# Kernel tuning notes

Measured on AMD Instinct MI355X. Metric: run time of the kernel, lower is better.

## Reference

```python
import jax, jax.numpy as jnp
import numpy as np

CR = 32  # channels // reduction

def setup_inputs() -> dict:
    key = jax.random.key(0)
    k1, k2 = jax.random.split(key)
    x = jax.random.normal(k1, (1, 64, 8, 32, 32), dtype=jnp.float32)
    W = jax.random.normal(k2, (CR, 64), dtype=jnp.float32) * (1.0 / np.sqrt(64.0))
    bias = jnp.zeros((CR,), dtype=jnp.float32)
    return {"x": x, "W": W, "bias": bias}

def reference(x, W, bias):
    b, c, d, h, w = x.shape
    cr = W.shape[0]
    n = d * h * w
    # 1x1x1 Conv3d == per-voxel linear projection over channels
    x_red = jnp.einsum('oc,bcdhw->bodhw', W, x) + bias[None, :, None, None, None]
    q = x_red.reshape(b, cr, n)          # [b, cr, N]
    k = q                                 # shared projection (q == k)
    v = x.reshape(b, c, n)               # [b, c, N]
    # attn[b, i, j] = <q[:, i], k[:, j]>, softmax over j (dim=2)
    attn = jnp.einsum('bci,bcj->bij', q, k) / jnp.sqrt(jnp.float32(cr))
    attn = jax.nn.softmax(attn, axis=2)
    # out[b, c, m] = sum_n v[b, c, n] * attn[b, n, m]  (torch.bmm(v, attn))
    out = jnp.einsum('bcn,bnm->bcm', v, attn)
    out = out.reshape(b, c, d, h, w)
    return out + x
```

## Files before the change

kernel.cpp:

```cpp
#include <hip/hip_runtime.h>

#define N_TOK 8192

typedef _Float16 f16x8 __attribute__((ext_vector_type(8)));
typedef _Float16 f16x4 __attribute__((ext_vector_type(4)));
typedef float    f32x4 __attribute__((ext_vector_type(4)));

__device__ __forceinline__ f32x4 mfma16(f16x8 a, f16x8 b, f32x4 c) {
  return __builtin_amdgcn_mfma_f32_16x16x32_f16(a, b, c, 0, 0, 0);
}

#define QSCALE 0.50500977f

__global__ __launch_bounds__(256) void prep_kernel(
    const float* __restrict__ x, const float* __restrict__ W,
    const float* __restrict__ bias, _Float16* __restrict__ qe,
    _Float16* __restrict__ vh) {
  int blk = blockIdx.x, t = threadIdx.x;
  if (blk < 1024) {
    __shared__ float Wl[32 * 65];
    for (int i = t; i < 2048; i += 256) Wl[(i >> 6) * 65 + (i & 63)] = W[i];
    __syncthreads();
    int g = blk * 256 + t;
    int o = g & 31, n = g >> 5;
    float acc0 = bias[o], acc1 = 0.f;
#pragma unroll
    for (int c = 0; c < 32; ++c) {
      acc0 = fmaf(Wl[o * 65 + c], x[c * N_TOK + n], acc0);
      acc1 = fmaf(Wl[o * 65 + 32 + c], x[(32 + c) * N_TOK + n], acc1);
    }
    qe[n * 32 + o] = (_Float16)((acc0 + acc1) * QSCALE);
  } else {
    int i4 = (blk - 1024) * 256 + t;
    f32x4 v = ((const f32x4*)x)[i4];
    f16x4 h;
#pragma unroll
    for (int j = 0; j < 4; ++j) h[j] = (_Float16)v[j];
    *(f16x4*)(vh + i4 * 4) = h;
  }
}

__global__ __launch_bounds__(512) void pass1_kernel(
    const _Float16* __restrict__ qe, float* __restrict__ Bn) {
  __shared__ float Lp[8][32];
  int t = threadIdx.x;
  int w = t >> 6, lane = t & 63, quad = lane >> 4, l15 = lane & 15;
  int n0 = blockIdx.x * 32;
  f16x8 af0 = *(const f16x8*)(qe + (n0 + l15) * 32 + quad * 8);
  f16x8 af1 = *(const f16x8*)(qe + (n0 + 16 + l15) * 32 + quad * 8);
  f32x4 sums0 = {0.f, 0.f, 0.f, 0.f}, sums1 = {0.f, 0.f, 0.f, 0.f};
  for (int mt = 0; mt < 64; ++mt) {
    int m0 = w * 1024 + mt * 16;
    f16x8 bf = *(const f16x8*)(qe + (m0 + l15) * 32 + quad * 8);
    f32x4 zero = {0.f, 0.f, 0.f, 0.f};
    f32x4 s0 = mfma16(af0, bf, zero);
    f32x4 s1 = mfma16(af1, bf, zero);
#pragma unroll
    for (int r = 0; r < 4; ++r) {
      sums0[r] += __builtin_amdgcn_exp2f(s0[r]);
      sums1[r] += __builtin_amdgcn_exp2f(s1[r]);
    }
  }
#pragma unroll
  for (int r = 0; r < 4; ++r) {
#pragma unroll
    for (int mask = 1; mask < 16; mask <<= 1) {
      sums0[r] += __shfl_xor(sums0[r], mask, 64);
      sums1[r] += __shfl_xor(sums1[r], mask, 64);
    }
  }
  if (l15 == 0) {
    *(f32x4*)&Lp[w][quad * 4] = sums0;
    *(f32x4*)&Lp[w][16 + quad * 4] = sums1;
  }
  __syncthreads();
  if (t < 32) {
    float L = 0.f;
#pragma unroll
    for (int ww = 0; ww < 8; ++ww) L += Lp[ww][t];
    Bn[n0 + t] = __builtin_amdgcn_logf(L);
  }
}

__global__ __launch_bounds__(1024) void pass2_kernel(
    const _Float16* __restrict__ qe, const _Float16* __restrict__ vh,
    const float* __restrict__ Bn, const float* __restrict__ x,
    float* __restrict__ out) {
  __shared__ _Float16 Pt[16 * 1280];
  __shared__ float Ot[8 * 64 * 33];
  int t = threadIdx.x;
  int w = t >> 6, lane = t & 63, quad = lane >> 4, l15 = lane & 15;
  int m0 = blockIdx.x * 32;
  _Float16* myP = Pt + w * 1280;

  f16x8 bm0 = *(const f16x8*)(qe + (m0 + l15) * 32 + quad * 8);
  f16x8 bm1 = *(const f16x8*)(qe + (m0 + 16 + l15) * 32 + quad * 8);

  f32x4 acc[4][2];
#pragma unroll
  for (int ct = 0; ct < 4; ++ct)
#pragma unroll
    for (int mt = 0; mt < 2; ++mt) acc[ct][mt] = f32x4{0.f, 0.f, 0.f, 0.f};

  for (int ch = 0; ch < 16; ++ch) {
    int nb = w * 512 + ch * 32;
    f16x8 an[2];
    an[0] = *(const f16x8*)(qe + (nb + l15) * 32 + quad * 8);
    an[1] = *(const f16x8*)(qe + (nb + 16 + l15) * 32 + quad * 8);
    f32x4 Bq[2];
    Bq[0] = *(const f32x4*)(Bn + nb + quad * 4);
    Bq[1] = *(const f32x4*)(Bn + nb + 16 + quad * 4);
    __asm__ volatile("s_waitcnt lgkmcnt(0)" ::: "memory");
#pragma unroll
    for (int nt = 0; nt < 2; ++nt) {
      f16x8 a = an[nt];
#pragma unroll
      for (int mt = 0; mt < 2; ++mt) {
        f32x4 zero = {0.f, 0.f, 0.f, 0.f};
        f32x4 s = mfma16(a, (mt == 0) ? bm0 : bm1, zero);
        f16x4 p;
#pragma unroll
        for (int r = 0; r < 4; ++r)
          p[r] = (_Float16)__builtin_amdgcn_exp2f(s[r] - Bq[nt][r]);
        *(f16x4*)(myP + (mt * 16 + l15) * 40 + nt * 16 + quad * 4) = p;
      }
    }
    __asm__ volatile("s_waitcnt lgkmcnt(0)" ::: "memory");
    f16x8 bp0 = *(const f16x8*)(myP + l15 * 40 + quad * 8);
    f16x8 bp1 = *(const f16x8*)(myP + (16 + l15) * 40 + quad * 8);
#pragma unroll
    for (int ct = 0; ct < 4; ++ct) {
      f16x8 av = *(const f16x8*)(vh + (ct * 16 + l15) * N_TOK + nb + quad * 8);
      acc[ct][0] = mfma16(av, bp0, acc[ct][0]);
      acc[ct][1] = mfma16(av, bp1, acc[ct][1]);
    }
  }

  if (w < 8) {
#pragma unroll
    for (int ct = 0; ct < 4; ++ct)
#pragma unroll
      for (int mt = 0; mt < 2; ++mt)
#pragma unroll
        for (int r = 0; r < 4; ++r)
          Ot[(w * 64 + ct * 16 + quad * 4 + r) * 33 + mt * 16 + l15] =
              acc[ct][mt][r];
  }
  __syncthreads();
  if (w >= 8) {
#pragma unroll
    for (int ct = 0; ct < 4; ++ct)
#pragma unroll
      for (int mt = 0; mt < 2; ++mt)
#pragma unroll
        for (int r = 0; r < 4; ++r)
          Ot[((w - 8) * 64 + ct * 16 + quad * 4 + r) * 33 + mt * 16 + l15] +=
              acc[ct][mt][r];
  }
  __syncthreads();
  for (int idx = t; idx < 2048; idx += 1024) {
    int cc = idx >> 5, m = idx & 31;
    float v = 0.f;
#pragma unroll
    for (int s = 0; s < 8; ++s) v += Ot[(s * 64 + cc) * 33 + m];
    out[cc * N_TOK + m0 + m] = v + x[cc * N_TOK + m0 + m];
  }
}

extern "C" void kernel_launch(void* const* d_in, const int* in_sizes, int n_in,
                              void* d_out, int out_size, void* d_ws,
                              size_t ws_size, hipStream_t stream) {
  const float* x = (const float*)d_in[0];
  const float* W = (const float*)d_in[1];
  const float* bias = (const float*)d_in[2];
  float* out = (float*)d_out;

  char* ws = (char*)d_ws;
  _Float16* qe = (_Float16*)ws;
  _Float16* vh = (_Float16*)(ws + 524288);
  float* Bn = (float*)(ws + 524288 + 1048576);

  prep_kernel<<<1536, 256, 0, stream>>>(x, W, bias, qe, vh);
  pass1_kernel<<<256, 512, 0, stream>>>(qe, Bn);
  pass2_kernel<<<256, 1024, 0, stream>>>(qe, vh, Bn, x, out);
}
```

Before: 113.9 us.

## Fuse prep and both attention passes into one cooperative kernel with grid syncs

Merges the three launches (projection/convert, log-sum-exp pass, output pass) into a single cooperative kernel of 256 blocks of 1024 threads, separated by grid-wide syncs. V is stored in a pre-permuted fp16 layout so the output pass can feed probabilities straight from the score MFMA registers into 16x16x16 MFMAs, removing the LDS round trip for P. Both passes also prefetch their next operand tiles into registers. The aim is to cut launch gaps and LDS traffic, at the cost of grid-sync overhead and a requirement that all 256 blocks be co-resident.

```diff
diff --git a/kernel.cpp b/kernel.cpp
--- a/kernel.cpp
+++ b/kernel.cpp
@@ -1,27 +1,39 @@
 #include <hip/hip_runtime.h>
+#include <hip/hip_cooperative_groups.h>
+
+namespace cg = cooperative_groups;
 
 #define N_TOK 8192
 
 typedef _Float16 f16x8 __attribute__((ext_vector_type(8)));
 typedef _Float16 f16x4 __attribute__((ext_vector_type(4)));
+typedef _Float16 f16x2 __attribute__((ext_vector_type(2)));
 typedef float    f32x4 __attribute__((ext_vector_type(4)));
 
-__device__ __forceinline__ f32x4 mfma16(f16x8 a, f16x8 b, f32x4 c) {
+__device__ __forceinline__ f32x4 mfma_k32(f16x8 a, f16x8 b, f32x4 c) {
   return __builtin_amdgcn_mfma_f32_16x16x32_f16(a, b, c, 0, 0, 0);
 }
+__device__ __forceinline__ f32x4 mfma_k16(f16x4 a, f16x4 b, f32x4 c) {
+  return __builtin_amdgcn_mfma_f32_16x16x16f16(a, b, c, 0, 0, 0);
+}
 
 #define QSCALE 0.50500977f
 
-__global__ __launch_bounds__(256) void prep_kernel(
+__global__ __launch_bounds__(1024, 4) void mega_kernel(
     const float* __restrict__ x, const float* __restrict__ W,
     const float* __restrict__ bias, _Float16* __restrict__ qe,
-    _Float16* __restrict__ vh) {
-  int blk = blockIdx.x, t = threadIdx.x;
-  if (blk < 1024) {
-    __shared__ float Wl[32 * 65];
-    for (int i = t; i < 2048; i += 256) Wl[(i >> 6) * 65 + (i & 63)] = W[i];
-    __syncthreads();
-    int g = blk * 256 + t;
+    _Float16* __restrict__ vp, float* __restrict__ Bn,
+    float* __restrict__ out) {
+  __shared__ float smem[8 * 64 * 33];
+  cg::grid_group grid = cg::this_grid();
+  int t = threadIdx.x, blk = blockIdx.x;
+  int w = t >> 6, lane = t & 63, quad = lane >> 4, l15 = lane & 15;
+
+  {
+    float* Wl = smem;
+    for (int i = t; i < 2048; i += 1024) Wl[(i >> 6) * 65 + (i & 63)] = W[i];
+    __syncthreads();
+    int g = blk * 1024 + t;
     int o = g & 31, n = g >> 5;
     float acc0 = bias[o], acc1 = 0.f;
 #pragma unroll
@@ -30,140 +42,157 @@
       acc1 = fmaf(Wl[o * 65 + 32 + c], x[(32 + c) * N_TOK + n], acc1);
     }
     qe[n * 32 + o] = (_Float16)((acc0 + acc1) * QSCALE);
-  } else {
-    int i4 = (blk - 1024) * 256 + t;
-    f32x4 v = ((const f32x4*)x)[i4];
-    f16x4 h;
-#pragma unroll
-    for (int j = 0; j < 4; ++j) h[j] = (_Float16)v[j];
-    *(f16x4*)(vh + i4 * 4) = h;
+    int f = g * 2;
+    int c = f >> 13, n2 = f & 8191;
+    float2 xv = *(const float2*)(x + f);
+    int gg = n2 >> 5, off = n2 & 31;
+    int nt = off >> 4, q2 = (off >> 2) & 3, j = off & 3;
+    f16x2 h;
+    h[0] = (_Float16)xv.x;
+    h[1] = (_Float16)xv.y;
+    *(f16x2*)(vp + ((gg * 64 + c) * 4 + q2) * 8 + nt * 4 + j) = h;
   }
-}
-
-__global__ __launch_bounds__(512) void pass1_kernel(
-    const _Float16* __restrict__ qe, float* __restrict__ Bn) {
-  __shared__ float Lp[8][32];
-  int t = threadIdx.x;
-  int w = t >> 6, lane = t & 63, quad = lane >> 4, l15 = lane & 15;
-  int n0 = blockIdx.x * 32;
-  f16x8 af0 = *(const f16x8*)(qe + (n0 + l15) * 32 + quad * 8);
-  f16x8 af1 = *(const f16x8*)(qe + (n0 + 16 + l15) * 32 + quad * 8);
-  f32x4 sums0 = {0.f, 0.f, 0.f, 0.f}, sums1 = {0.f, 0.f, 0.f, 0.f};
-  for (int mt = 0; mt < 64; ++mt) {
-    int m0 = w * 1024 + mt * 16;
-    f16x8 bf = *(const f16x8*)(qe + (m0 + l15) * 32 + quad * 8);
-    f32x4 zero = {0.f, 0.f, 0.f, 0.f};
-    f32x4 s0 = mfma16(af0, bf, zero);
-    f32x4 s1 = mfma16(af1, bf, zero);
+  grid.sync();
+
+  {
+    float(*Lp)[32] = reinterpret_cast<float(*)[32]>(smem);
+    int n0 = blk * 32;
+    f16x8 af0 = *(const f16x8*)(qe + (n0 + l15) * 32 + quad * 8);
+    f16x8 af1 = *(const f16x8*)(qe + (n0 + 16 + l15) * 32 + quad * 8);
+    const _Float16* qb = qe + (w * 512 + l15) * 32 + quad * 8;
+    f16x8 pb0 = *(const f16x8*)(qb);
+    f16x8 pb1 = *(const f16x8*)(qb + 512);
+    f32x4 a00 = {0.f, 0.f, 0.f, 0.f}, a01 = a00, a10 = a00, a11 = a00;
+    for (int mt = 0; mt < 16; ++mt) {
+      f16x8 b0 = pb0, b1 = pb1;
+      int nx = ((mt + 1) & 15) * 1024;
+      pb0 = *(const f16x8*)(qb + nx);
+      pb1 = *(const f16x8*)(qb + nx + 512);
+      f32x4 z = {0.f, 0.f, 0.f, 0.f};
+      f32x4 s00 = mfma_k32(af0, b0, z);
+      f32x4 s01 = mfma_k32(af0, b1, z);
+      f32x4 s10 = mfma_k32(af1, b0, z);
+      f32x4 s11 = mfma_k32(af1, b1, z);
+#pragma unroll
+      for (int r = 0; r < 4; ++r) {
+        a00[r] += __builtin_amdgcn_exp2f(s00[r]);
+        a01[r] += __builtin_amdgcn_exp2f(s01[r]);
+        a10[r] += __builtin_amdgcn_exp2f(s10[r]);
+        a11[r] += __builtin_amdgcn_exp2f(s11[r]);
+      }
+    }
+    f32x4 sums0 = a00 + a01;
+    f32x4 sums1 = a10 + a11;
 #pragma unroll
     for (int r = 0; r < 4; ++r) {
-      sums0[r] += __builtin_amdgcn_exp2f(s0[r]);
-      sums1[r] += __builtin_amdgcn_exp2f(s1[r]);
+#pragma unroll
+      for (int mask = 1; mask < 16; mask <<= 1) {
+        sums0[r] += __shfl_xor(sums0[r], mask, 64);
+        sums1[r] += __shfl_xor(sums1[r], mask, 64);
+      }
+    }
+    if (l15 == 0) {
+      *(f32x4*)&Lp[w][quad * 4] = sums0;
+      *(f32x4*)&Lp[w][16 + quad * 4] = sums1;
+    }
+    __syncthreads();
+    if (t < 32) {
+      float L = 0.f;
+#pragma unroll
+      for (int ww = 0; ww < 16; ++ww) L += Lp[ww][t];
+      Bn[n0 + t] = __builtin_amdgcn_logf(L);
     }
   }
-#pragma unroll
-  for (int r = 0; r < 4; ++r) {
-#pragma unroll
-    for (int mask = 1; mask < 16; mask <<= 1) {
-      sums0[r] += __shfl_xor(sums0[r], mask, 64);
-      sums1[r] += __shfl_xor(sums1[r], mask, 64);
-    }
-  }
-  if (l15 == 0) {
-    *(f32x4*)&Lp[w][quad * 4] = sums0;
-    *(f32x4*)&Lp[w][16 + quad * 4] = sums1;
-  }
-  __syncthreads();
-  if (t < 32) {
-    float L = 0.f;
-#pragma unroll
-    for (int ww = 0; ww < 8; ++ww) L += Lp[ww][t];
-    Bn[n0 + t] = __builtin_amdgcn_logf(L);
-  }
-}
-
-__global__ __launch_bounds__(1024) void pass2_kernel(
-    const _Float16* __restrict__ qe, const _Float16* __restrict__ vh,
-    const float* __restrict__ Bn, const float* __restrict__ x,
-    float* __restrict__ out) {
-  __shared__ _Float16 Pt[16 * 1280];
-  __shared__ float Ot[8 * 64 * 33];
-  int t = threadIdx.x;
-  int w = t >> 6, lane = t & 63, quad = lane >> 4, l15 = lane & 15;
-  int m0 = blockIdx.x * 32;
-  _Float16* myP = Pt + w * 1280;
-
-  f16x8 bm0 = *(const f16x8*)(qe + (m0 + l15) * 32 + quad * 8);
-  f16x8 bm1 = *(const f16x8*)(qe + (m0 + 16 + l15) * 32 + quad * 8);
-
-  f32x4 acc[4][2];
-#pragma unroll
-  for (int ct = 0; ct < 4; ++ct)
-#pragma unroll
-    for (int mt = 0; mt < 2; ++mt) acc[ct][mt] = f32x4{0.f, 0.f, 0.f, 0.f};
-
-  for (int ch = 0; ch < 16; ++ch) {
-    int nb = w * 512 + ch * 32;
-    f16x8 an[2];
-    an[0] = *(const f16x8*)(qe + (nb + l15) * 32 + quad * 8);
-    an[1] = *(const f16x8*)(qe + (nb + 16 + l15) * 32 + quad * 8);
-    f32x4 Bq[2];
-    Bq[0] = *(const f32x4*)(Bn + nb + quad * 4);
-    Bq[1] = *(const f32x4*)(Bn + nb + 16 + quad * 4);
-    __asm__ volatile("s_waitcnt lgkmcnt(0)" ::: "memory");
-#pragma unroll
-    for (int nt = 0; nt < 2; ++nt) {
-      f16x8 a = an[nt];
-#pragma unroll
-      for (int mt = 0; mt < 2; ++mt) {
-        f32x4 zero = {0.f, 0.f, 0.f, 0.f};
-        f32x4 s = mfma16(a, (mt == 0) ? bm0 : bm1, zero);
-        f16x4 p;
-#pragma unroll
-        for (int r = 0; r < 4; ++r)
-          p[r] = (_Float16)__builtin_amdgcn_exp2f(s[r] - Bq[nt][r]);
-        *(f16x4*)(myP + (mt * 16 + l15) * 40 + nt * 16 + quad * 4) = p;
-      }
-    }
-    __asm__ volatile("s_waitcnt lgkmcnt(0)" ::: "memory");
-    f16x8 bp0 = *(const f16x8*)(myP + l15 * 40 + quad * 8);
-    f16x8 bp1 = *(const f16x8*)(myP + (16 + l15) * 40 + quad * 8);
-#pragma unroll
-    for (int ct = 0; ct < 4; ++ct) {
-      f16x8 av = *(const f16x8*)(vh + (ct * 16 + l15) * N_TOK + nb + quad * 8);
-      acc[ct][0] = mfma16(av, bp0, acc[ct][0]);
-      acc[ct][1] = mfma16(av, bp1, acc[ct][1]);
-    }
-  }
-
-  if (w < 8) {
+  grid.sync();
+
+  {
+    float* Ot = smem;
+    int m0 = blk * 32;
+    f16x8 bm0 = *(const f16x8*)(qe + (m0 + l15) * 32 + quad * 8);
+    f16x8 bm1 = *(const f16x8*)(qe + (m0 + 16 + l15) * 32 + quad * 8);
+
+    int base = w * 512;
+    const _Float16* qa = qe + (base + l15) * 32 + quad * 8;
+    const float* bnb = Bn + base + quad * 4;
+
+    f32x4 acc[4][2];
 #pragma unroll
     for (int ct = 0; ct < 4; ++ct)
 #pragma unroll
-      for (int mt = 0; mt < 2; ++mt)
-#pragma unroll
-        for (int r = 0; r < 4; ++r)
-          Ot[(w * 64 + ct * 16 + quad * 4 + r) * 33 + mt * 16 + l15] =
-              acc[ct][mt][r];
-  }
-  __syncthreads();
-  if (w >= 8) {
-#pragma unroll
-    for (int ct = 0; ct < 4; ++ct)
-#pragma unroll
-      for (int mt = 0; mt < 2; ++mt)
-#pragma unroll
-        for (int r = 0; r < 4; ++r)
-          Ot[((w - 8) * 64 + ct * 16 + quad * 4 + r) * 33 + mt * 16 + l15] +=
-              acc[ct][mt][r];
-  }
-  __syncthreads();
-  for (int idx = t; idx < 2048; idx += 1024) {
-    int cc = idx >> 5, m = idx & 31;
-    float v = 0.f;
-#pragma unroll
-    for (int s = 0; s < 8; ++s) v += Ot[(s * 64 + cc) * 33 + m];
-    out[cc * N_TOK + m0 + m] = v + x[cc * N_TOK + m0 + m];
+      for (int mt = 0; mt < 2; ++mt) acc[ct][mt] = f32x4{0.f, 0.f, 0.f, 0.f};
+
+    f16x8 an[2][2];
+    an[0][0] = *(const f16x8*)(qa);
+    an[0][1] = *(const f16x8*)(qa + 512);
+
+#pragma unroll 2
+    for (int ch = 0; ch < 16; ++ch) {
+      int cur = ch & 1, nxt = cur ^ 1;
+      int nb = base + ch * 32;
+      f32x4 Bq0 = *(const f32x4*)(bnb + ch * 32);
+      f32x4 Bq1 = *(const f32x4*)(bnb + ch * 32 + 16);
+      f16x8 av8[4];
+#pragma unroll
+      for (int ct = 0; ct < 4; ++ct)
+        av8[ct] = *(const f16x8*)(vp + (((nb >> 5) * 64 + ct * 16 + l15) * 4 +
+                                        quad) * 8);
+      int rnx = ((ch + 1) & 15) * 32;
+      an[nxt][0] = *(const f16x8*)(qa + rnx * 32);
+      an[nxt][1] = *(const f16x8*)(qa + rnx * 32 + 512);
+
+      f32x4 z = {0.f, 0.f, 0.f, 0.f};
+      f32x4 s00 = mfma_k32(an[cur][0], bm0, z);
+      f32x4 s01 = mfma_k32(an[cur][0], bm1, z);
+      f32x4 s10 = mfma_k32(an[cur][1], bm0, z);
+      f32x4 s11 = mfma_k32(an[cur][1], bm1, z);
+      f16x4 p00, p01, p10, p11;
+#pragma unroll
+      for (int r = 0; r < 4; ++r) {
+        p00[r] = (_Float16)__builtin_amdgcn_exp2f(s00[r] - Bq0[r]);
+        p01[r] = (_Float16)__builtin_amdgcn_exp2f(s01[r] - Bq0[r]);
+        p10[r] = (_Float16)__builtin_amdgcn_exp2f(s10[r] - Bq1[r]);
+        p11[r] = (_Float16)__builtin_amdgcn_exp2f(s11[r] - Bq1[r]);
+      }
+#pragma unroll
+      for (int ct = 0; ct < 4; ++ct) {
+        f16x4 lo = __builtin_shufflevector(av8[ct], av8[ct], 0, 1, 2, 3);
+        f16x4 hi = __builtin_shufflevector(av8[ct], av8[ct], 4, 5, 6, 7);
+        acc[ct][0] = mfma_k16(lo, p00, acc[ct][0]);
+        acc[ct][1] = mfma_k16(lo, p01, acc[ct][1]);
+        acc[ct][0] = mfma_k16(hi, p10, acc[ct][0]);
+        acc[ct][1] = mfma_k16(hi, p11, acc[ct][1]);
+      }
+    }
+
+    if (w < 8) {
+#pragma unroll
+      for (int ct = 0; ct < 4; ++ct)
+#pragma unroll
+        for (int mt = 0; mt < 2; ++mt)
+#pragma unroll
+          for (int r = 0; r < 4; ++r)
+            Ot[(w * 64 + ct * 16 + quad * 4 + r) * 33 + mt * 16 + l15] =
+                acc[ct][mt][r];
+    }
+    __syncthreads();
+    if (w >= 8) {
+#pragma unroll
+      for (int ct = 0; ct < 4; ++ct)
+#pragma unroll
+        for (int mt = 0; mt < 2; ++mt)
+#pragma unroll
+          for (int r = 0; r < 4; ++r)
+            Ot[((w - 8) * 64 + ct * 16 + quad * 4 + r) * 33 + mt * 16 + l15] +=
+                acc[ct][mt][r];
+    }
+    __syncthreads();
+    for (int idx = t; idx < 2048; idx += 1024) {
+      int cc = idx >> 5, m = idx & 31;
+      float v = 0.f;
+#pragma unroll
+      for (int s = 0; s < 8; ++s) v += Ot[(s * 64 + cc) * 33 + m];
+      out[cc * N_TOK + m0 + m] = v + x[cc * N_TOK + m0 + m];
+    }
   }
 }
 
@@ -177,10 +206,11 @@
 
   char* ws = (char*)d_ws;
   _Float16* qe = (_Float16*)ws;
-  _Float16* vh = (_Float16*)(ws + 524288);
+  _Float16* vp = (_Float16*)(ws + 524288);
   float* Bn = (float*)(ws + 524288 + 1048576);
 
-  prep_kernel<<<1536, 256, 0, stream>>>(x, W, bias, qe, vh);
-  pass1_kernel<<<256, 512, 0, stream>>>(qe, Bn);
-  pass2_kernel<<<256, 1024, 0, stream>>>(qe, vh, Bn, x, out);
-}
+  void* args[] = {(void*)&x,  (void*)&W,  (void*)&bias, (void*)&qe,
+                  (void*)&vp, (void*)&Bn, (void*)&out};
+  hipLaunchCooperativeKernel((void*)mega_kernel, dim3(256), dim3(1024), args,
+                             0, stream);
+}
```

Result: slower. 190.5 us (+67.3%).
